# Performance work log

Measured on AMD Instinct MI355X. Metric: run time of the kernel, lower is better.

The kernel has to match this reference:

```python
import jax, jax.numpy as jnp
import numpy as np

B, C_H, C_L = 8, 128, 256
H_H, W_H = 64, 64
H_L, W_L = 128, 128
CS = 8
K = CS * CS  # 64 external keys (== inter_channels, matches hardcoded reatt dim)
EPS = 1e-5


def _bn(x, g, b, m, v):
    # inference-mode BatchNorm2d over channel dim 1
    scale = g / jnp.sqrt(v + EPS)
    return (x - m[None, :, None, None]) * scale[None, :, None, None] + b[None, :, None, None]


def setup_inputs() -> dict:
    key = jax.random.key(0)
    ks = jax.random.split(key, 13)
    return {
        "x_h": jax.random.normal(ks[0], (B, C_H, H_H, W_H), jnp.float32),
        "x_l": jax.random.normal(ks[1], (B, C_L, H_L, W_L), jnp.float32),
        "bn_h_gamma": jax.random.normal(ks[2], (C_H,), jnp.float32),
        "bn_h_beta": jax.random.normal(ks[3], (C_H,), jnp.float32),
        "bn_h_mean": jax.random.normal(ks[4], (C_H,), jnp.float32),
        "bn_h_var": jax.random.uniform(ks[5], (C_H,), jnp.float32),
        "kv_w": jax.random.normal(ks[6], (2 * C_L, C_H), jnp.float32) * 0.05,
        "kv_b": jax.random.normal(ks[7], (2 * C_L,), jnp.float32) * 0.05,
        "bn_l_gamma": jax.random.normal(ks[8], (C_L,), jnp.float32),
        "bn_l_beta": jax.random.normal(ks[9], (C_L,), jnp.float32),
        "bn_l_mean": jax.random.normal(ks[10], (C_L,), jnp.float32),
        "bn_l_var": jax.random.uniform(ks[11], (C_L,), jnp.float32),
        "reatt": jax.random.normal(ks[12], (1, K, 1, 1), jnp.float32) * 1e-5,
    }


def reference(x_h, x_l, bn_h_gamma, bn_h_beta, bn_h_mean, bn_h_var,
              kv_w, kv_b, bn_l_gamma, bn_l_beta, bn_l_mean, bn_l_var, reatt):
    # ---- cross_kv: BN -> AdaptiveMaxPool2d(8,8) -> 1x1 conv ----
    xh = _bn(x_h, bn_h_gamma, bn_h_beta, bn_h_mean, bn_h_var)
    # exact window max pool (H_H, W_H divisible by CS)
    p = xh.reshape(B, C_H, CS, H_H // CS, CS, W_H // CS).max(axis=(3, 5))  # [B,C_H,8,8]
    kv = jnp.einsum('bchw,oc->bohw', p, kv_w) + kv_b[None, :, None, None]  # [B,2*C_L,8,8]
    ck = kv[:, :C_L]   # [B,C_L,8,8]
    cv = kv[:, C_L:]   # [B,C_L,8,8]
    # cross_k: permute NHWC then flatten -> per-sample [K, C_L] key matrix
    ck = ck.transpose(0, 2, 3, 1).reshape(B, K, C_L)
    # cross_v: flatten spatial -> per-sample [C_L, K] value matrix
    cv = cv.reshape(B, C_L, K)

    # ---- ExternalAttention (use_cross_kv path) ----
    xl = _bn(x_l, bn_l_gamma, bn_l_beta, bn_l_mean, bn_l_var)
    # grouped 1x1 conv (groups=B) == per-sample projection onto K external keys
    attn = jnp.einsum('bchw,bkc->bkhw', xl, ck)          # [B,K,H_L,W_L]
    attn = attn + reatt                                   # broadcast [1,K,1,1]
    # _act_sn: scale by inter_channels^-0.5, softmax over the K key channels
    attn = jax.nn.softmax(attn * (K ** -0.5), axis=1)
    # grouped 1x1 conv with values: per-sample [C_L,K] @ [K,H*W]
    out = jnp.einsum('bkhw,bck->bchw', attn, cv)          # [B,C_L,H_L,W_L]
    return x_l + out
```

## Files before the change

kernel.cpp:

```cpp
#include <hip/hip_runtime.h>
#include <math.h>

#define B_     8
#define C_H_   128
#define C_L_   256
#define K_     64
#define NPIX_L 16384
#define EPS_   1e-5f

#define P_OFF     0
#define P_SZ      (B_*K_*C_H_)
#define B1_BYTE   (P_SZ*4)
#define B2_BYTE   (B1_BYTE + B_*K_*C_L_*2)
#define BIAS_BYTE (B2_BYTE + B_*K_*C_L_*2)

typedef short bf16x8 __attribute__((ext_vector_type(8)));
typedef float f32x4  __attribute__((ext_vector_type(4)));

__device__ inline unsigned short f2bf(float f) {
    unsigned int u = __float_as_uint(f);
    u += 0x7FFFu + ((u >> 16) & 1u);
    return (unsigned short)(u >> 16);
}
__device__ inline unsigned int pack2bf(float lo, float hi) {
    unsigned int ul = __float_as_uint(lo);
    unsigned int uh = __float_as_uint(hi);
    ul = (ul + (0x7FFFu + ((ul >> 16) & 1u))) >> 16;
    uh = (uh + (0x7FFFu + ((uh >> 16) & 1u))) & 0xFFFF0000u;
    return ul | uh;
}

#define MFMA16(a, b, c) __builtin_amdgcn_mfma_f32_16x16x32_bf16((a), (b), (c), 0, 0, 0)

#define GLOAD_LDS16(g, l) __builtin_amdgcn_global_load_lds( \
    (const __attribute__((address_space(1))) void*)(g), \
    (__attribute__((address_space(3))) void*)(l), 16, 0, 0)

__global__ __launch_bounds__(256) void pool_bn_kernel(
    const float* __restrict__ x_h,
    const float* __restrict__ g, const float* __restrict__ be,
    const float* __restrict__ mn, const float* __restrict__ vr,
    float* __restrict__ ws)
{
    const int t   = threadIdx.x;
    const int k   = t & 63;
    const int cl  = t >> 6;
    const int bid = blockIdx.x;
    const int b   = bid >> 5;
    const int c   = ((bid & 31) << 2) + cl;

    const float* plane = x_h + ((size_t)(b * C_H_ + c) << 12);
    const int ph = k >> 3, pw = k & 7;
    const float* p0 = plane + (ph * 8) * 64 + pw * 8;

    float mx = -INFINITY, mnv = INFINITY;
#pragma unroll
    for (int i = 0; i < 8; i++) {
        const float4 a  = *reinterpret_cast<const float4*>(p0 + i * 64);
        const float4 bq = *reinterpret_cast<const float4*>(p0 + i * 64 + 4);
        mx  = fmaxf(mx,  fmaxf(fmaxf(a.x, a.y),  fmaxf(a.z, a.w)));
        mx  = fmaxf(mx,  fmaxf(fmaxf(bq.x, bq.y), fmaxf(bq.z, bq.w)));
        mnv = fminf(mnv, fminf(fminf(a.x, a.y),  fminf(a.z, a.w)));
        mnv = fminf(mnv, fminf(fminf(bq.x, bq.y), fminf(bq.z, bq.w)));
    }
    const float sc  = g[c] * rsqrtf(vr[c] + EPS_);
    const float sel = (sc >= 0.f) ? mx : mnv;
    ws[P_OFF + (b * K_ + k) * C_H_ + c] = fmaf(sel - mn[c], sc, be[c]);
}

__global__ __launch_bounds__(256) void kv_kernel(
    const float* __restrict__ kv_w, const float* __restrict__ kv_b,
    const float* __restrict__ lg, const float* __restrict__ lb,
    const float* __restrict__ lm, const float* __restrict__ lv,
    const float* __restrict__ ratt,
    float* __restrict__ ws)
{
    __shared__ __align__(16) float prow[C_H_];
    __shared__ float red[4];
    const int t   = threadIdx.x;
    const int bid = blockIdx.x;
    const int b   = bid >> 6;
    const int kk  = bid & 63;

    if (t < C_H_ / 4) {
        reinterpret_cast<float4*>(prow)[t] =
            reinterpret_cast<const float4*>(ws + P_OFF + (b * K_ + kk) * C_H_)[t];
    }
    __syncthreads();

    float a0 = kv_b[t];
    float a1 = kv_b[t + 256];
    const float* w0 = kv_w + (size_t)t * C_H_;
    const float* w1 = kv_w + (size_t)(t + 256) * C_H_;
#pragma unroll
    for (int c = 0; c < C_H_; c += 4) {
        const float4 pv  = *reinterpret_cast<const float4*>(prow + c);
        const float4 wv0 = *reinterpret_cast<const float4*>(w0 + c);
        const float4 wv1 = *reinterpret_cast<const float4*>(w1 + c);
        a0 = fmaf(wv0.x, pv.x, a0); a0 = fmaf(wv0.y, pv.y, a0);
        a0 = fmaf(wv0.z, pv.z, a0); a0 = fmaf(wv0.w, pv.w, a0);
        a1 = fmaf(wv1.x, pv.x, a1); a1 = fmaf(wv1.y, pv.y, a1);
        a1 = fmaf(wv1.z, pv.z, a1); a1 = fmaf(wv1.w, pv.w, a1);
    }

    const float s = lg[t] * rsqrtf(lv[t] + EPS_);
    const float h = fmaf(-lm[t], s, lb[t]);

    float contrib = h * a0;
#pragma unroll
    for (int m = 1; m < 64; m <<= 1) contrib += __shfl_xor(contrib, m, 64);
    if ((t & 63) == 0) red[t >> 6] = contrib;
    __syncthreads();

    unsigned short* b1 = (unsigned short*)((char*)ws + B1_BYTE);
    unsigned short* b2 = (unsigned short*)((char*)ws + B2_BYTE);

    {
        const int s1 = t >> 5, j = t & 7;
        const int l  = ((t >> 3) & 3) * 16 + (kk & 15);
        const int n  = kk >> 4;
        b1[((((b * 8 + s1) * 4 + n) * 64) + l) * 8 + j] = f2bf(a0 * s);
    }
    {
        const int s2 = kk >> 5, j2 = kk & 7;
        const int l2 = ((kk >> 3) & 3) * 16 + (t & 15);
        const int n2 = t >> 4;
        b2[((((b * 2 + s2) * 16 + n2) * 64) + l2) * 8 + j2] = f2bf(a1);
    }
    if (t == 0) {
        float* bia = (float*)((char*)ws + BIAS_BYTE);
        bia[b * K_ + kk] = (red[0] + red[1] + red[2] + red[3] + ratt[kk]) * 0.125f;
    }
}

__global__ __launch_bounds__(256, 4) void attn_mfma(
    const float* __restrict__ x_l,
    const float* __restrict__ ws_f,
    float* __restrict__ out)
{
    __shared__ __align__(16) char lds[33280];
    float* xbuf0 = (float*)lds;
    float* xbuf1 = (float*)(lds + 16384);
    unsigned short* wscr = (unsigned short*)lds;
    float* obuf = (float*)(lds + 16384);

    const int t    = threadIdx.x;
    const int lane = t & 63;
    const int wid  = t >> 6;
    const int bid  = blockIdx.x;
    const int b    = bid & 7;
    const int tile = bid >> 3;
    const int px0  = tile * 128;
    const int pxw  = wid * 32;
    const int r16  = lane & 15;
    const int q    = lane >> 4;

    const unsigned short* b1 = (const unsigned short*)((const char*)ws_f + B1_BYTE);
    const unsigned short* b2 = (const unsigned short*)((const char*)ws_f + B2_BYTE);
    const float* biasf = (const float*)((const char*)ws_f + BIAS_BYTE) + b * K_;
    const float* xb = x_l + (size_t)b * (C_L_ * NPIX_L);
    float* ob = out + (size_t)b * (C_L_ * NPIX_L);

    float bl[4];
#pragma unroll
    for (int n = 0; n < 4; n++) bl[n] = biasf[16 * n + r16];

    const int su = ((lane & 31) ^ (wid << 2)) << 2;
    const int sd = lane >> 5;
#define STAGE(bufp, s_) do { \
    _Pragma("unroll") \
    for (int i_ = 0; i_ < 4; i_++) { \
        const int cl_ = 8 * wid + 2 * i_; \
        const float* gp_ = xb + (size_t)(32 * (s_) + cl_ + sd) * NPIX_L + px0 + su; \
        GLOAD_LDS16(gp_, (bufp) + (size_t)cl_ * 128); \
    } \
} while (0)

    f32x4 acc1[2][4] = {};
    union ABu { bf16x8 v; unsigned int u[4]; };

    STAGE(xbuf0, 0);

    const int p0x = (pxw + r16) ^ (q << 4);
    const int p1x = (pxw + 16 + r16) ^ (q << 4);

#pragma unroll
    for (int s = 0; s < 8; s++) {
        float* xbf = (s & 1) ? xbuf1 : xbuf0;
        if (s < 7) {
            STAGE((s & 1) ? xbuf0 : xbuf1, s + 1);
            asm volatile("s_waitcnt vmcnt(4)" ::: "memory");
        } else {
            asm volatile("s_waitcnt vmcnt(0)" ::: "memory");
        }
        __builtin_amdgcn_s_barrier();

        ABu a0f, a1f;
#pragma unroll
        for (int jj = 0; jj < 4; jj++) {
            const float* row0 = xbf + (8 * q + 2 * jj) * 128;
            const float* row1 = xbf + (8 * q + 2 * jj + 1) * 128;
            a0f.u[jj] = pack2bf(row0[p0x], row1[p0x]);
            a1f.u[jj] = pack2bf(row0[p1x], row1[p1x]);
        }
        const bf16x8* bp = ((const bf16x8*)b1) + ((b * 8 + s) * 4) * 64 + lane;
#pragma unroll
        for (int n = 0; n < 4; n++) {
            const bf16x8 bfr = bp[n * 64];
            acc1[0][n] = MFMA16(a0f.v, bfr, acc1[0][n]);
            acc1[1][n] = MFMA16(a1f.v, bfr, acc1[1][n]);
        }
        __builtin_amdgcn_s_barrier();
    }

    unsigned short* wsb = wscr + wid * 1152;
    bf16x8 af[2][2];
#pragma unroll
    for (int m = 0; m < 2; m++) {
#pragma unroll
        for (int r = 0; r < 4; r++) {
            float e0 = fmaf(acc1[m][0][r], 0.125f, bl[0]);
            float e1 = fmaf(acc1[m][1][r], 0.125f, bl[1]);
            float e2 = fmaf(acc1[m][2][r], 0.125f, bl[2]);
            float e3 = fmaf(acc1[m][3][r], 0.125f, bl[3]);
            float mx = fmaxf(fmaxf(e0, e1), fmaxf(e2, e3));
#pragma unroll
            for (int msk = 1; msk < 16; msk <<= 1) mx = fmaxf(mx, __shfl_xor(mx, msk, 64));
            e0 = __expf(e0 - mx); e1 = __expf(e1 - mx);
            e2 = __expf(e2 - mx); e3 = __expf(e3 - mx);
            float sm = (e0 + e1) + (e2 + e3);
#pragma unroll
            for (int msk = 1; msk < 16; msk <<= 1) sm += __shfl_xor(sm, msk, 64);
            const float inv = 1.f / sm;
            unsigned short* wp = wsb + (q * 4 + r) * 72 + r16;
            wp[0]  = f2bf(e0 * inv);
            wp[16] = f2bf(e1 * inv);
            wp[32] = f2bf(e2 * inv);
            wp[48] = f2bf(e3 * inv);
        }
#pragma unroll
        for (int s2 = 0; s2 < 2; s2++)
            af[m][s2] = *(const bf16x8*)(wsb + r16 * 72 + 32 * s2 + q * 8);
        if (m == 0) asm volatile("s_waitcnt lgkmcnt(0)" ::: "memory");
    }

#pragma unroll
    for (int nc = 0; nc < 4; nc++) {
        f32x4 acc2[2][4] = {};
#pragma unroll
        for (int s2 = 0; s2 < 2; s2++) {
            const bf16x8* bp2 = ((const bf16x8*)b2) + ((b * 2 + s2) * 16 + nc * 4) * 64 + lane;
#pragma unroll
            for (int nn = 0; nn < 4; nn++) {
                const bf16x8 bfr = bp2[nn * 64];
                acc2[0][nn] = MFMA16(af[0][s2], bfr, acc2[0][nn]);
                acc2[1][nn] = MFMA16(af[1][s2], bfr, acc2[1][nn]);
            }
        }
#pragma unroll
        for (int h = 0; h < 2; h++) {
#pragma unroll
            for (int m = 0; m < 2; m++)
#pragma unroll
                for (int e = 0; e < 2; e++) {
                    float* dp = obuf + (16 * e + r16) * 132 + (pxw + 16 * m + 4 * q);
                    *(f32x4*)dp = acc2[m][2 * h + e];
                }
            asm volatile("s_waitcnt lgkmcnt(0)" ::: "memory");
            __builtin_amdgcn_s_barrier();
            const int cbase = 64 * nc + 32 * h;
#pragma unroll
            for (int u2 = 0; u2 < 4; u2++) {
                const int idx = t + 256 * u2;
                const int col = idx >> 5;
                const int un  = idx & 31;
                const float4 vv = *(const float4*)(obuf + col * 132 + un * 4);
                const size_t gbase = (size_t)(cbase + col) * NPIX_L + px0 + un * 4;
                const float4 xv4 = *(const float4*)(xb + gbase);
                float4 o;
                o.x = vv.x + xv4.x; o.y = vv.y + xv4.y;
                o.z = vv.z + xv4.z; o.w = vv.w + xv4.w;
                *(float4*)(ob + gbase) = o;
            }
            __builtin_amdgcn_s_barrier();
        }
    }
#undef STAGE
}

extern "C" void kernel_launch(void* const* d_in, const int* in_sizes, int n_in,
                              void* d_out, int out_size, void* d_ws, size_t ws_size,
                              hipStream_t stream) {
    const float* x_h  = (const float*)d_in[0];
    const float* x_l  = (const float*)d_in[1];
    const float* hg   = (const float*)d_in[2];
    const float* hb   = (const float*)d_in[3];
    const float* hm   = (const float*)d_in[4];
    const float* hv   = (const float*)d_in[5];
    const float* kvw  = (const float*)d_in[6];
    const float* kvb  = (const float*)d_in[7];
    const float* lg   = (const float*)d_in[8];
    const float* lb   = (const float*)d_in[9];
    const float* lm   = (const float*)d_in[10];
    const float* lv   = (const float*)d_in[11];
    const float* ratt = (const float*)d_in[12];
    float* ws  = (float*)d_ws;
    float* out = (float*)d_out;

    pool_bn_kernel<<<256, 256, 0, stream>>>(x_h, hg, hb, hm, hv, ws);
    kv_kernel<<<512, 256, 0, stream>>>(kvw, kvb, lg, lb, lm, lv, ratt, ws);
    attn_mfma<<<1024, 256, 0, stream>>>(x_l, ws, out);
}
```

Before: 306.6 us.

## Restructure kv projection to reuse weights across four key rows per block

The kv projection kernel now has each block handle four pooled key rows and half the output channels, so each weight float4 load is reused for four dot products. Each reduction is split across four lanes and combined with shuffles. The grid shrinks from 512 to 256 blocks. This cuts redundant global weight traffic in a small prologue kernel, at the cost of extra shuffles and more register use per thread. Overall the gain is likely small because the attention kernel dominates runtime.

```diff
diff --git a/kernel.cpp b/kernel.cpp
--- a/kernel.cpp
+++ b/kernel.cpp
@@ -75,61 +75,88 @@
     const float* __restrict__ ratt,
     float* __restrict__ ws)
 {
-    __shared__ __align__(16) float prow[C_H_];
-    __shared__ float red[4];
-    const int t   = threadIdx.x;
-    const int bid = blockIdx.x;
-    const int b   = bid >> 6;
-    const int kk  = bid & 63;
-
-    if (t < C_H_ / 4) {
-        reinterpret_cast<float4*>(prow)[t] =
-            reinterpret_cast<const float4*>(ws + P_OFF + (b * K_ + kk) * C_H_)[t];
+    __shared__ __align__(16) float plds[4 * 132];
+    __shared__ float red[4][4];
+    const int t    = threadIdx.x;
+    const int lane = t & 63;
+    const int wid  = t >> 6;
+    const int bid  = blockIdx.x;
+    const int b    = bid >> 5;
+    const int kg   = (bid >> 1) & 15;
+    const int oh   = bid & 1;
+
+    if (t < 128) {
+        const int px = t >> 5, u = t & 31;
+        const float4 v = *reinterpret_cast<const float4*>(
+            ws + P_OFF + (size_t)(b * K_ + kg * 4 + px) * C_H_ + u * 4);
+        *reinterpret_cast<float4*>(plds + px * 132 + u * 4) = v;
     }
     __syncthreads();
 
-    float a0 = kv_b[t];
-    float a1 = kv_b[t + 256];
-    const float* w0 = kv_w + (size_t)t * C_H_;
-    const float* w1 = kv_w + (size_t)(t + 256) * C_H_;
-#pragma unroll
-    for (int c = 0; c < C_H_; c += 4) {
-        const float4 pv  = *reinterpret_cast<const float4*>(prow + c);
-        const float4 wv0 = *reinterpret_cast<const float4*>(w0 + c);
-        const float4 wv1 = *reinterpret_cast<const float4*>(w1 + c);
-        a0 = fmaf(wv0.x, pv.x, a0); a0 = fmaf(wv0.y, pv.y, a0);
-        a0 = fmaf(wv0.z, pv.z, a0); a0 = fmaf(wv0.w, pv.w, a0);
-        a1 = fmaf(wv1.x, pv.x, a1); a1 = fmaf(wv1.y, pv.y, a1);
-        a1 = fmaf(wv1.z, pv.z, a1); a1 = fmaf(wv1.w, pv.w, a1);
-    }
-
-    const float s = lg[t] * rsqrtf(lv[t] + EPS_);
-    const float h = fmaf(-lm[t], s, lb[t]);
-
-    float contrib = h * a0;
-#pragma unroll
-    for (int m = 1; m < 64; m <<= 1) contrib += __shfl_xor(contrib, m, 64);
-    if ((t & 63) == 0) red[t >> 6] = contrib;
-    __syncthreads();
+    const int oi = t >> 2;
+    const int q4 = t & 3;
+    const int kk = kg * 4 + q4;
 
     unsigned short* b1 = (unsigned short*)((char*)ws + B1_BYTE);
     unsigned short* b2 = (unsigned short*)((char*)ws + B2_BYTE);
 
-    {
-        const int s1 = t >> 5, j = t & 7;
-        const int l  = ((t >> 3) & 3) * 16 + (kk & 15);
-        const int n  = kk >> 4;
-        b1[((((b * 8 + s1) * 4 + n) * 64) + l) * 8 + j] = f2bf(a0 * s);
-    }
-    {
-        const int s2 = kk >> 5, j2 = kk & 7;
-        const int l2 = ((kk >> 3) & 3) * 16 + (t & 15);
-        const int n2 = t >> 4;
-        b2[((((b * 2 + s2) * 16 + n2) * 64) + l2) * 8 + j2] = f2bf(a1);
-    }
-    if (t == 0) {
-        float* bia = (float*)((char*)ws + BIAS_BYTE);
-        bia[b * K_ + kk] = (red[0] + red[1] + red[2] + red[3] + ratt[kk]) * 0.125f;
+    float bc = 0.f;
+#pragma unroll
+    for (int pass = 0; pass < 4; pass++) {
+        const int o = oh * 256 + pass * 64 + oi;
+        const float* wrow = kv_w + (size_t)o * C_H_ + q4 * 4;
+        float a0 = 0.f, a1 = 0.f, a2 = 0.f, a3 = 0.f;
+#pragma unroll
+        for (int i = 0; i < 8; i++) {
+            const float4 wf = *reinterpret_cast<const float4*>(wrow + i * 16);
+            const float4 p0 = *reinterpret_cast<const float4*>(plds + 0 * 132 + i * 16 + q4 * 4);
+            const float4 p1 = *reinterpret_cast<const float4*>(plds + 1 * 132 + i * 16 + q4 * 4);
+            const float4 p2 = *reinterpret_cast<const float4*>(plds + 2 * 132 + i * 16 + q4 * 4);
+            const float4 p3 = *reinterpret_cast<const float4*>(plds + 3 * 132 + i * 16 + q4 * 4);
+            a0 = fmaf(wf.x, p0.x, a0); a0 = fmaf(wf.y, p0.y, a0);
+            a0 = fmaf(wf.z, p0.z, a0); a0 = fmaf(wf.w, p0.w, a0);
+            a1 = fmaf(wf.x, p1.x, a1); a1 = fmaf(wf.y, p1.y, a1);
+            a1 = fmaf(wf.z, p1.z, a1); a1 = fmaf(wf.w, p1.w, a1);
+            a2 = fmaf(wf.x, p2.x, a2); a2 = fmaf(wf.y, p2.y, a2);
+            a2 = fmaf(wf.z, p2.z, a2); a2 = fmaf(wf.w, p2.w, a2);
+            a3 = fmaf(wf.x, p3.x, a3); a3 = fmaf(wf.y, p3.y, a3);
+            a3 = fmaf(wf.z, p3.z, a3); a3 = fmaf(wf.w, p3.w, a3);
+        }
+        a0 += __shfl_xor(a0, 1, 64); a0 += __shfl_xor(a0, 2, 64);
+        a1 += __shfl_xor(a1, 1, 64); a1 += __shfl_xor(a1, 2, 64);
+        a2 += __shfl_xor(a2, 1, 64); a2 += __shfl_xor(a2, 2, 64);
+        a3 += __shfl_xor(a3, 1, 64); a3 += __shfl_xor(a3, 2, 64);
+        float val = (q4 == 0) ? a0 : (q4 == 1) ? a1 : (q4 == 2) ? a2 : a3;
+        val += kv_b[o];
+
+        if (oh == 0) {
+            const float s = lg[o] * rsqrtf(lv[o] + EPS_);
+            const float h = fmaf(-lm[o], s, lb[o]);
+            bc = fmaf(h, val, bc);
+            const int s1 = o >> 5, j = o & 7;
+            const int l  = ((o >> 3) & 3) * 16 + (kk & 15);
+            const int n  = kk >> 4;
+            b1[((((b * 8 + s1) * 4 + n) * 64) + l) * 8 + j] = f2bf(val * s);
+        } else {
+            const int co = o - 256;
+            const int s2 = kk >> 5, j2 = kk & 7;
+            const int l2 = ((kk >> 3) & 3) * 16 + (co & 15);
+            const int n2 = co >> 4;
+            b2[((((b * 2 + s2) * 16 + n2) * 64) + l2) * 8 + j2] = f2bf(val);
+        }
+    }
+
+    if (oh == 0) {
+#pragma unroll
+        for (int m = 4; m < 64; m <<= 1) bc += __shfl_xor(bc, m, 64);
+        if (lane < 4) red[wid][lane] = bc;
+        __syncthreads();
+        if (t < 4) {
+            const float sum = red[0][t] + red[1][t] + red[2][t] + red[3][t];
+            const int kkf = kg * 4 + t;
+            float* bia = (float*)((char*)ws + BIAS_BYTE);
+            bia[b * K_ + kkf] = (sum + ratt[kkf]) * 0.125f;
+        }
     }
 }
 
@@ -308,6 +335,6 @@
     float* out = (float*)d_out;
 
     pool_bn_kernel<<<256, 256, 0, stream>>>(x_h, hg, hb, hm, hv, ws);
-    kv_kernel<<<512, 256, 0, stream>>>(kvw, kvb, lg, lb, lm, lv, ratt, ws);
+    kv_kernel<<<256, 256, 0, stream>>>(kvw, kvb, lg, lb, lm, lv, ratt, ws);
     attn_mfma<<<1024, 256, 0, stream>>>(x_l, ws, out);
 }
```

New measurement: 302.7 us. No clear change (-1.3%).
